# Kernel optimization log

Measured on AMD Instinct MI355X. Metric: run time of the kernel, lower is better.

Reference implementation:

```python
import jax, jax.numpy as jnp
import numpy as np

EMBED_DIM = 1024
NUM_HEADS = 16
HEAD_DIM = EMBED_DIM // NUM_HEADS
SCALING = HEAD_DIM ** (-0.5)
SEQ = 2048
BSZ = 2


def setup_inputs() -> dict:
    key = jax.random.key(0)
    ks = jax.random.split(key, 11)
    d = {
        "query": jax.random.normal(ks[0], (SEQ, BSZ, EMBED_DIM), dtype=jnp.float32),
        "key": jax.random.normal(ks[1], (SEQ, BSZ, EMBED_DIM), dtype=jnp.float32),
        "value": jax.random.normal(ks[2], (SEQ, BSZ, EMBED_DIM), dtype=jnp.float32),
        "bias_q": jax.random.normal(ks[3], (SEQ, EMBED_DIM), dtype=jnp.float32),
        "bias_k": jax.random.normal(ks[4], (SEQ, EMBED_DIM), dtype=jnp.float32),
        "bias_v": jax.random.normal(ks[5], (SEQ, EMBED_DIM), dtype=jnp.float32),
        # Linear weights (out, in); xavier-ish scale
        "Wq": jax.random.normal(ks[6], (EMBED_DIM, EMBED_DIM), dtype=jnp.float32) * (1.0 / np.sqrt(2 * EMBED_DIM)),
        "Wk": jax.random.normal(ks[7], (EMBED_DIM, EMBED_DIM), dtype=jnp.float32) * (1.0 / np.sqrt(2 * EMBED_DIM)),
        "Wv": jax.random.normal(ks[8], (EMBED_DIM, EMBED_DIM), dtype=jnp.float32) * (1.0 / np.sqrt(2 * EMBED_DIM)),
        "Wo": jax.random.normal(ks[9], (EMBED_DIM, EMBED_DIM), dtype=jnp.float32) * (1.0 / np.sqrt(EMBED_DIM)),
        "bo": jnp.zeros((EMBED_DIM,), dtype=jnp.float32),
    }
    return d


def reference(query, key, value, bias_q, bias_k, bias_v, Wq, Wk, Wv, Wo, bo):
    tgt_len, bsz, embed_dim = query.shape
    # self_attention=True: q, k, v all projected from `query`
    q = (query @ Wq.T + bias_q[:, None, :]) * SCALING   # [T,B,E]
    k = query @ Wk.T + bias_k[:, None, :]                # [T,B,E]
    v = query @ Wv.T + bias_v[:, None, :]                # [T,B,E]

    def split_heads(x):  # [T,B,E] -> [B*H, T, Dh]
        return x.reshape(tgt_len, bsz * NUM_HEADS, HEAD_DIM).transpose(1, 0, 2)

    q, k, v = split_heads(q), split_heads(k), split_heads(v)
    attn_weights = jnp.einsum('btd,bsd->bts', q, k)      # [B*H, T, S]
    attn_weights = jax.nn.softmax(attn_weights, axis=-1)
    attn = jnp.einsum('bts,bsd->btd', attn_weights, v)   # [B*H, T, Dh]
    attn = attn.transpose(1, 0, 2).reshape(tgt_len, bsz, embed_dim)
    attn = attn @ Wo.T + bo
    return (attn, attn_weights)
```

## Files before the change

### kernel.cpp

```cpp
#include <hip/hip_runtime.h>
#include <hip/hip_fp16.h>
#include <cmath>

#define SEQLEN 2048
#define BATCH 2
#define EMB 1024
#define NHEAD 16
#define DHEAD 64
#define NBH 32
#define NROWS 4096

typedef _Float16 f16;
typedef __attribute__((ext_vector_type(4))) _Float16 f16x4;
typedef __attribute__((ext_vector_type(8))) _Float16 f16x8;
typedef __attribute__((ext_vector_type(4))) float f32x4;

__device__ __forceinline__ void gload_lds16(const f16* g, f16* l) {
    __builtin_amdgcn_global_load_lds(
        (const __attribute__((address_space(1))) void*)g,
        (__attribute__((address_space(3))) void*)l, 16, 0, 0);
}

#define QN4 1048576
#define WN4 262144
__global__ __launch_bounds__(256) void cvt_all_kernel(
    const float* __restrict__ query, const float* __restrict__ w0,
    const float* __restrict__ w1, const float* __restrict__ w2,
    const float* __restrict__ w3,
    f16* __restrict__ xh, f16* __restrict__ o0, f16* __restrict__ o1,
    f16* __restrict__ o2, f16* __restrict__ o3)
{
    const int total = QN4 + 4 * WN4;
    for (int i = blockIdx.x * 256 + threadIdx.x; i < total; i += 2048 * 256) {
        const float* src; f16* dst; int off;
        if (i < QN4) { src = query; dst = xh; off = i; }
        else {
            int j = i - QN4;
            int sel = j >> 18;
            off = j & (WN4 - 1);
            switch (sel) {
                case 0: src = w0; dst = o0; break;
                case 1: src = w1; dst = o1; break;
                case 2: src = w2; dst = o2; break;
                default: src = w3; dst = o3; break;
            }
        }
        float4 v = reinterpret_cast<const float4*>(src)[off];
        f16x4 o = {(_Float16)v.x, (_Float16)v.y, (_Float16)v.z, (_Float16)v.w};
        reinterpret_cast<f16x4*>(dst)[off] = o;
    }
}

#define PBK 32

__global__ __launch_bounds__(256, 3) void proj_kernel(
    const f16* __restrict__ xh,
    const f16* __restrict__ Wqh, const f16* __restrict__ Wkh, const f16* __restrict__ Wvh,
    const float* __restrict__ bq, const float* __restrict__ bk, const float* __restrict__ bv,
    f16* __restrict__ qh, f16* __restrict__ kh, f16* __restrict__ vT)
{
    __shared__ __align__(16) f16 smem[16384];

    const int c0f = blockIdx.y * 128;
    const int mode = c0f >> 10;
    const int c0 = c0f & 1023;
    const f16* __restrict__ W = (mode == 0) ? Wqh : (mode == 1 ? Wkh : Wvh);
    const float* __restrict__ bias = (mode == 0) ? bq : (mode == 1 ? bk : bv);
    const int r0 = blockIdx.x * 128;
    const int w = threadIdx.x >> 6;
    const int lane = threadIdx.x & 63;
    const int lr = lane & 15, lg = lane >> 4;
    const int wr = w >> 1, wc = w & 1;

    const int cA0 = w * 64 + lane;
    const int cA1 = 256 + w * 64 + lane;
    const f16* gA0 = xh + (size_t)(r0 + (cA0 >> 2)) * EMB + (cA0 & 3) * 8;
    const f16* gA1 = xh + (size_t)(r0 + (cA1 >> 2)) * EMB + (cA1 & 3) * 8;
    const f16* gB0 = W + (size_t)(c0 + (cA0 >> 2)) * EMB + (cA0 & 3) * 8;
    const f16* gB1 = W + (size_t)(c0 + (cA1 >> 2)) * EMB + (cA1 & 3) * 8;
    const int lds0 = (w * 64) * 8;
    const int lds1 = (256 + w * 64) * 8;

    f32x4 acc[4][4] = {};
    int cur = 0;

    gload_lds16(gA0, smem + lds0);
    gload_lds16(gA1, smem + lds1);
    gload_lds16(gB0, smem + 8192 + lds0);
    gload_lds16(gB1, smem + 8192 + lds1);
    __syncthreads();

    for (int kt = 0; kt < EMB / PBK; ++kt) {
        if (kt + 1 < EMB / PBK) {
            const int ko = (kt + 1) * PBK;
            const int nxt = (cur ^ 1) * 4096;
            gload_lds16(gA0 + ko, smem + nxt + lds0);
            gload_lds16(gA1 + ko, smem + nxt + lds1);
            gload_lds16(gB0 + ko, smem + 8192 + nxt + lds0);
            gload_lds16(gB1 + ko, smem + 8192 + nxt + lds1);
        }
        const f16* Ac = smem + cur * 4096;
        const f16* Bc = smem + 8192 + cur * 4096;
        f16x8 a[4], b[4];
#pragma unroll
        for (int m = 0; m < 4; ++m)
            a[m] = *reinterpret_cast<const f16x8*>(
                &Ac[(wr * 64 + m * 16 + lr) * PBK + lg * 8]);
#pragma unroll
        for (int n = 0; n < 4; ++n)
            b[n] = *reinterpret_cast<const f16x8*>(
                &Bc[(wc * 64 + n * 16 + lr) * PBK + lg * 8]);
#pragma unroll
        for (int m = 0; m < 4; ++m)
#pragma unroll
            for (int n = 0; n < 4; ++n)
                acc[m][n] = __builtin_amdgcn_mfma_f32_16x16x32_f16(b[n], a[m], acc[m][n], 0, 0, 0);
        __syncthreads();
        cur ^= 1;
    }

    if (mode != 2) {
        f16* __restrict__ dst = (mode == 0) ? qh : kh;
        const float sc = (mode == 0) ? 0.125f : 1.0f;
#pragma unroll
        for (int m = 0; m < 4; ++m) {
            const int row = r0 + wr * 64 + m * 16 + lr;
            const int t = row >> 1, bb = row & 1;
#pragma unroll
            for (int n = 0; n < 4; ++n) {
                const int col0 = c0 + wc * 64 + n * 16 + lg * 4;
                float4 b4 = *reinterpret_cast<const float4*>(&bias[(size_t)t * EMB + col0]);
                f16x4 pk = {(_Float16)((acc[m][n][0] + b4.x) * sc),
                            (_Float16)((acc[m][n][1] + b4.y) * sc),
                            (_Float16)((acc[m][n][2] + b4.z) * sc),
                            (_Float16)((acc[m][n][3] + b4.w) * sc)};
                const int h = col0 >> 6, d0 = col0 & 63;
                const int bhi = bb * NHEAD + h;
                *reinterpret_cast<f16x4*>(
                    &dst[((size_t)bhi * SEQLEN + t) * DHEAD + d0]) = pk;
            }
        }
    } else {
        f16* T = smem;
#pragma unroll
        for (int p = 0; p < 2; ++p) {
            if (wr == p) {
#pragma unroll
                for (int m = 0; m < 4; ++m) {
                    const int row = r0 + p * 64 + m * 16 + lr;
                    const int t = row >> 1;
#pragma unroll
                    for (int n = 0; n < 4; ++n) {
                        const int ci0 = wc * 64 + n * 16 + lg * 4;
                        float4 b4 = *reinterpret_cast<const float4*>(
                            &bias[(size_t)t * EMB + c0 + ci0]);
                        f16x4 pk = {(_Float16)(acc[m][n][0] + b4.x),
                                    (_Float16)(acc[m][n][1] + b4.y),
                                    (_Float16)(acc[m][n][2] + b4.z),
                                    (_Float16)(acc[m][n][3] + b4.w)};
                        *reinterpret_cast<f16x4*>(&T[(m * 16 + lr) * 132 + ci0]) = pk;
                    }
                }
            }
            __syncthreads();
            {
                const int dd = threadIdx.x & 63;
                const int hh = (threadIdx.x >> 6) & 1;
                const int bb2 = threadIdx.x >> 7;
                const int bhi2 = bb2 * NHEAD + ((c0 + hh * 64) >> 6);
                const int tbase = (r0 + p * 64) >> 1;
                f16* __restrict__ vrow =
                    vT + ((size_t)bhi2 * 64 + (tbase >> 5)) * (DHEAD * 32) + dd * 32;
#pragma unroll
                for (int j8 = 0; j8 < 4; ++j8) {
                    f16x8 pk8;
#pragma unroll
                    for (int jj = 0; jj < 8; ++jj)
                        pk8[jj] = T[(bb2 + 2 * (j8 * 8 + jj)) * 132 + hh * 64 + dd];
                    *reinterpret_cast<f16x8*>(&vrow[j8 * 8]) = pk8;
                }
            }
            __syncthreads();
        }
    }
}

#define QBLK 16
#define SCHUNK 256
#define TPITCH 264
#define RPITCH 1040

__global__ __launch_bounds__(512, 4) void attn_kernel(
    const f16* __restrict__ qh, const f16* __restrict__ kh, const f16* __restrict__ vT,
    float* __restrict__ Pout, f16* __restrict__ ctx)
{
    __shared__ __align__(16) f16 tbuf[8][QBLK * TPITCH];
    __shared__ float lsum[QBLK][8];
    __shared__ float inv_l[QBLK];
    float* red = (float*)&tbuf[0][0];

    const int id = blockIdx.x;
    const int idx = id >> 3;
    const int bh = ((id & 7) << 2) + (idx >> 7);
    const int t0 = (idx & 127) * QBLK;

    const int w = threadIdx.x >> 6;
    const int lane = threadIdx.x & 63;
    const int lr = lane & 15, lg = lane >> 4;
    const int sbase = w * SCHUNK;

    const f16* __restrict__ qb = qh + (size_t)bh * SEQLEN * DHEAD;
    const f16* __restrict__ kb = kh + (size_t)bh * SEQLEN * DHEAD;
    const f16* __restrict__ vb = vT + (size_t)bh * DHEAD * SEQLEN;

    f16x8 qf[2];
#pragma unroll
    for (int kc = 0; kc < 2; ++kc)
        qf[kc] = *reinterpret_cast<const f16x8*>(
            qb + (size_t)(t0 + lr) * DHEAD + kc * 32 + lg * 8);

    f16x4 ev[16];
    float rowsum = 0.f;
#pragma unroll
    for (int st = 0; st < 16; ++st) {
        const f16* krow = kb + (size_t)(sbase + st * 16 + lr) * DHEAD;
        f16x8 kf0 = *reinterpret_cast<const f16x8*>(krow + lg * 8);
        f16x8 kf1 = *reinterpret_cast<const f16x8*>(krow + 32 + lg * 8);
        f32x4 sa = {};
        sa = __builtin_amdgcn_mfma_f32_16x16x32_f16(kf0, qf[0], sa, 0, 0, 0);
        sa = __builtin_amdgcn_mfma_f32_16x16x32_f16(kf1, qf[1], sa, 0, 0, 0);
        float ps = 0.f;
#pragma unroll
        for (int e = 0; e < 4; ++e) {
            float Ev = __expf(sa[e]) * 0.0625f;
            ev[st][e] = (_Float16)Ev;
            ps += Ev;
        }
        rowsum += ps;
    }

    {
        float v = rowsum;
        v += __shfl_xor(v, 16);
        v += __shfl_xor(v, 32);
        if (lg == 0) lsum[lr][w] = v;
    }

    f16* mybuf = &tbuf[w][0];
#pragma unroll
    for (int st = 0; st < 16; ++st)
        *reinterpret_cast<f16x4*>(&mybuf[lr * TPITCH + st * 16 + lg * 4]) = ev[st];

    __syncthreads();
    if (threadIdx.x < QBLK) {
        float s = 0.f;
#pragma unroll
        for (int i = 0; i < 8; ++i) s += lsum[threadIdx.x][i];
        inv_l[threadIdx.x] = 1.0f / s;
    }
    __syncthreads();

    float* __restrict__ Pt =
        Pout + (size_t)bh * SEQLEN * SEQLEN + (size_t)t0 * SEQLEN;
#pragma unroll
    for (int j = 0; j < 2; ++j) {
        const int t = w * 2 + j;
        const float inv = inv_l[t];
#pragma unroll
        for (int c = 0; c < 8; ++c) {
            f16x4 e4 = *reinterpret_cast<const f16x4*>(
                &tbuf[c][t * TPITCH + lane * 4]);
            f32x4 o = {(float)e4[0] * inv, (float)e4[1] * inv,
                       (float)e4[2] * inv, (float)e4[3] * inv};
            __builtin_nontemporal_store(o,
                reinterpret_cast<f32x4*>(&Pt[(size_t)t * SEQLEN + c * SCHUNK + lane * 4]));
        }
    }

    f32x4 accO[4] = {};
#pragma unroll
    for (int c = 0; c < 8; ++c) {
        f16x8 pa = *reinterpret_cast<const f16x8*>(&mybuf[lr * TPITCH + c * 32 + lg * 8]);
        const f16* vchunk = vb + (size_t)(w * 8 + c) * (DHEAD * 32);
#pragma unroll
        for (int dt = 0; dt < 4; ++dt) {
            f16x8 vf = *reinterpret_cast<const f16x8*>(
                vchunk + (dt * 16 + lr) * 32 + lg * 8);
            accO[dt] = __builtin_amdgcn_mfma_f32_16x16x32_f16(pa, vf, accO[dt], 0, 0, 0);
        }
    }
    __syncthreads();

#pragma unroll
    for (int dt = 0; dt < 4; ++dt)
#pragma unroll
        for (int e = 0; e < 4; ++e)
            red[(size_t)w * RPITCH + (lg * 4 + e) * 65 + dt * 16 + lr] = accO[dt][e];
    __syncthreads();

    const int b = bh >> 4, h = bh & 15;
    for (int o = threadIdx.x; o < QBLK * DHEAD; o += 512) {
        const int t = o >> 6, d = o & 63;
        float s = 0.f;
#pragma unroll
        for (int i = 0; i < 8; ++i) s += red[(size_t)i * RPITCH + t * 65 + d];
        s *= inv_l[t];
        ctx[(size_t)((t0 + t) * BATCH + b) * EMB + h * DHEAD + d] = (f16)s;
    }
}

__global__ __launch_bounds__(256, 4) void oproj_kernel(
    const f16* __restrict__ ctx, const f16* __restrict__ Woh,
    const float* __restrict__ bo, float* __restrict__ out)
{
    __shared__ __align__(16) f16 smem[12288];
    const int r0 = blockIdx.x * 64;
    const int c0 = blockIdx.y * 128;
    const int w = threadIdx.x >> 6;
    const int lane = threadIdx.x & 63;
    const int lr = lane & 15, lg = lane >> 4;
    const int wr = w >> 1, wc = w & 1;

    const int cA = threadIdx.x;
    const f16* gA = ctx + (size_t)(r0 + (cA >> 2)) * EMB + (cA & 3) * 8;
    const f16* gB0 = Woh + (size_t)(c0 + (cA >> 2)) * EMB + (cA & 3) * 8;
    const f16* gB1 = Woh + (size_t)(c0 + 64 + (cA >> 2)) * EMB + (cA & 3) * 8;
    const int ldsA = (w * 64) * 8;
    const int ldsB0 = (w * 64) * 8;
    const int ldsB1 = (256 + w * 64) * 8;

    f32x4 acc[2][4] = {};
    int cur = 0;

    gload_lds16(gA, smem + ldsA);
    gload_lds16(gB0, smem + 4096 + ldsB0);
    gload_lds16(gB1, smem + 4096 + ldsB1);
    __syncthreads();

    for (int kt = 0; kt < EMB / PBK; ++kt) {
        if (kt + 1 < EMB / PBK) {
            const int ko = (kt + 1) * PBK;
            const int nxtA = (cur ^ 1) * 2048;
            const int nxtB = 4096 + (cur ^ 1) * 4096;
            gload_lds16(gA + ko, smem + nxtA + ldsA);
            gload_lds16(gB0 + ko, smem + nxtB + ldsB0);
            gload_lds16(gB1 + ko, smem + nxtB + ldsB1);
        }
        const f16* Ac = smem + cur * 2048;
        const f16* Bc = smem + 4096 + cur * 4096;
        f16x8 a[2], b[4];
#pragma unroll
        for (int m = 0; m < 2; ++m)
            a[m] = *reinterpret_cast<const f16x8*>(
                &Ac[(wr * 32 + m * 16 + lr) * PBK + lg * 8]);
#pragma unroll
        for (int n = 0; n < 4; ++n)
            b[n] = *reinterpret_cast<const f16x8*>(
                &Bc[(wc * 64 + n * 16 + lr) * PBK + lg * 8]);
#pragma unroll
        for (int m = 0; m < 2; ++m)
#pragma unroll
            for (int n = 0; n < 4; ++n)
                acc[m][n] = __builtin_amdgcn_mfma_f32_16x16x32_f16(b[n], a[m], acc[m][n], 0, 0, 0);
        __syncthreads();
        cur ^= 1;
    }

#pragma unroll
    for (int m = 0; m < 2; ++m) {
        const int row = r0 + wr * 32 + m * 16 + lr;
#pragma unroll
        for (int n = 0; n < 4; ++n) {
            const int col0 = c0 + wc * 64 + n * 16 + lg * 4;
            float4 b4 = *reinterpret_cast<const float4*>(&bo[col0]);
            f32x4 o = {acc[m][n][0] + b4.x, acc[m][n][1] + b4.y,
                       acc[m][n][2] + b4.z, acc[m][n][3] + b4.w};
            __builtin_nontemporal_store(o,
                reinterpret_cast<f32x4*>(&out[(size_t)row * EMB + col0]));
        }
    }
}

extern "C" void kernel_launch(void* const* d_in, const int* in_sizes, int n_in,
                              void* d_out, int out_size, void* d_ws, size_t ws_size,
                              hipStream_t stream) {
    const float* query = (const float*)d_in[0];
    const float* bq = (const float*)d_in[3];
    const float* bk = (const float*)d_in[4];
    const float* bv = (const float*)d_in[5];
    const float* Wq = (const float*)d_in[6];
    const float* Wk = (const float*)d_in[7];
    const float* Wv = (const float*)d_in[8];
    const float* Wo = (const float*)d_in[9];
    const float* bo = (const float*)d_in[10];

    char* ws = (char*)d_ws;
    f16* xh  = (f16*)(ws);
    f16* Wqh = (f16*)(ws + ( 8u << 20));
    f16* Wkh = (f16*)(ws + (10u << 20));
    f16* Wvh = (f16*)(ws + (12u << 20));
    f16* Woh = (f16*)(ws + (14u << 20));
    f16* qhp = (f16*)(ws + (16u << 20));
    f16* khp = (f16*)(ws + (24u << 20));
    f16* vTp = (f16*)(ws + (32u << 20));
    f16* ctx = (f16*)(ws + (40u << 20));

    float* outA = (float*)d_out;
    float* outP = (float*)d_out + (size_t)SEQLEN * BATCH * EMB;

    cvt_all_kernel<<<2048, 256, 0, stream>>>(query, Wq, Wk, Wv, Wo,
                                             xh, Wqh, Wkh, Wvh, Woh);

    proj_kernel<<<dim3(NROWS / 128, 3072 / 128), 256, 0, stream>>>(
        xh, Wqh, Wkh, Wvh, bq, bk, bv, qhp, khp, vTp);

    attn_kernel<<<SEQLEN / QBLK * NBH, 512, 0, stream>>>(qhp, khp, vTp, outP, ctx);

    oproj_kernel<<<dim3(NROWS / 64, EMB / 128), 256, 0, stream>>>(ctx, Woh, bo, outA);
}
```

Before: 264.6 us.

## Process 32 query rows per attention block with 16 waves sharing K/V loads

Doubles the query tile per block to 32 rows and splits the key range across 16 waves of 128 keys each, so every loaded K and V fragment feeds two MFMA query tiles. This is meant to cut global K/V reload traffic per query row. It raises LDS usage to about 139 KB and uses 1024-thread blocks, which limits occupancy to one block per CU. The cross-wave reduction of the output grows to 16 partials.

Result: faster. 228.1 us (median of 2 runs) (-13.8%).

```diff
diff --git a/kernel.cpp b/kernel.cpp
--- a/kernel.cpp
+++ b/kernel.cpp
@@ -185,24 +185,24 @@
     }
 }
 
-#define QBLK 16
-#define SCHUNK 256
-#define TPITCH 264
-#define RPITCH 1040
-
-__global__ __launch_bounds__(512, 4) void attn_kernel(
+#define QBLK 32
+#define SCHUNK 128
+#define TP 136
+#define RP 2080
+
+__global__ __launch_bounds__(1024, 1) void attn_kernel(
     const f16* __restrict__ qh, const f16* __restrict__ kh, const f16* __restrict__ vT,
     float* __restrict__ Pout, f16* __restrict__ ctx)
 {
-    __shared__ __align__(16) f16 tbuf[8][QBLK * TPITCH];
-    __shared__ float lsum[QBLK][8];
+    __shared__ __align__(16) f16 tbuf[16][QBLK * TP];
+    __shared__ float lsum[QBLK][16];
     __shared__ float inv_l[QBLK];
     float* red = (float*)&tbuf[0][0];
 
     const int id = blockIdx.x;
     const int idx = id >> 3;
-    const int bh = ((id & 7) << 2) + (idx >> 7);
-    const int t0 = (idx & 127) * QBLK;
+    const int bh = ((id & 7) << 2) + (idx >> 6);
+    const int t0 = (idx & 63) * QBLK;
 
     const int w = threadIdx.x >> 6;
     const int lane = threadIdx.x & 63;
@@ -213,49 +213,58 @@
     const f16* __restrict__ kb = kh + (size_t)bh * SEQLEN * DHEAD;
     const f16* __restrict__ vb = vT + (size_t)bh * DHEAD * SEQLEN;
 
-    f16x8 qf[2];
-#pragma unroll
-    for (int kc = 0; kc < 2; ++kc)
-        qf[kc] = *reinterpret_cast<const f16x8*>(
-            qb + (size_t)(t0 + lr) * DHEAD + kc * 32 + lg * 8);
-
-    f16x4 ev[16];
-    float rowsum = 0.f;
-#pragma unroll
-    for (int st = 0; st < 16; ++st) {
+    f16x8 qf[2][2];
+#pragma unroll
+    for (int tt = 0; tt < 2; ++tt)
+#pragma unroll
+        for (int kc = 0; kc < 2; ++kc)
+            qf[tt][kc] = *reinterpret_cast<const f16x8*>(
+                qb + (size_t)(t0 + tt * 16 + lr) * DHEAD + kc * 32 + lg * 8);
+
+    f16x4 ev[2][8];
+    float rowsum[2] = {0.f, 0.f};
+#pragma unroll
+    for (int st = 0; st < 8; ++st) {
         const f16* krow = kb + (size_t)(sbase + st * 16 + lr) * DHEAD;
         f16x8 kf0 = *reinterpret_cast<const f16x8*>(krow + lg * 8);
         f16x8 kf1 = *reinterpret_cast<const f16x8*>(krow + 32 + lg * 8);
-        f32x4 sa = {};
-        sa = __builtin_amdgcn_mfma_f32_16x16x32_f16(kf0, qf[0], sa, 0, 0, 0);
-        sa = __builtin_amdgcn_mfma_f32_16x16x32_f16(kf1, qf[1], sa, 0, 0, 0);
-        float ps = 0.f;
-#pragma unroll
-        for (int e = 0; e < 4; ++e) {
-            float Ev = __expf(sa[e]) * 0.0625f;
-            ev[st][e] = (_Float16)Ev;
-            ps += Ev;
-        }
-        rowsum += ps;
-    }
-
-    {
-        float v = rowsum;
+#pragma unroll
+        for (int tt = 0; tt < 2; ++tt) {
+            f32x4 sa = {};
+            sa = __builtin_amdgcn_mfma_f32_16x16x32_f16(kf0, qf[tt][0], sa, 0, 0, 0);
+            sa = __builtin_amdgcn_mfma_f32_16x16x32_f16(kf1, qf[tt][1], sa, 0, 0, 0);
+            float ps = 0.f;
+#pragma unroll
+            for (int e = 0; e < 4; ++e) {
+                float Ev = __expf(sa[e]) * 0.0625f;
+                ev[tt][st][e] = (_Float16)Ev;
+                ps += Ev;
+            }
+            rowsum[tt] += ps;
+        }
+    }
+
+#pragma unroll
+    for (int tt = 0; tt < 2; ++tt) {
+        float v = rowsum[tt];
         v += __shfl_xor(v, 16);
         v += __shfl_xor(v, 32);
-        if (lg == 0) lsum[lr][w] = v;
+        if (lg == 0) lsum[tt * 16 + lr][w] = v;
     }
 
     f16* mybuf = &tbuf[w][0];
 #pragma unroll
-    for (int st = 0; st < 16; ++st)
-        *reinterpret_cast<f16x4*>(&mybuf[lr * TPITCH + st * 16 + lg * 4]) = ev[st];
+    for (int tt = 0; tt < 2; ++tt)
+#pragma unroll
+        for (int st = 0; st < 8; ++st)
+            *reinterpret_cast<f16x4*>(
+                &mybuf[(tt * 16 + lr) * TP + st * 16 + lg * 4]) = ev[tt][st];
 
     __syncthreads();
     if (threadIdx.x < QBLK) {
         float s = 0.f;
 #pragma unroll
-        for (int i = 0; i < 8; ++i) s += lsum[threadIdx.x][i];
+        for (int i = 0; i < 16; ++i) s += lsum[threadIdx.x][i];
         inv_l[threadIdx.x] = 1.0f / s;
     }
     __syncthreads();
@@ -267,43 +276,50 @@
         const int t = w * 2 + j;
         const float inv = inv_l[t];
 #pragma unroll
-        for (int c = 0; c < 8; ++c) {
+        for (int cc = 0; cc < 8; ++cc) {
+            const int chunk = cc * 2 + (lane >> 5);
+            const int col = (lane & 31) * 4;
             f16x4 e4 = *reinterpret_cast<const f16x4*>(
-                &tbuf[c][t * TPITCH + lane * 4]);
+                &tbuf[chunk][t * TP + col]);
             f32x4 o = {(float)e4[0] * inv, (float)e4[1] * inv,
                        (float)e4[2] * inv, (float)e4[3] * inv};
             __builtin_nontemporal_store(o,
-                reinterpret_cast<f32x4*>(&Pt[(size_t)t * SEQLEN + c * SCHUNK + lane * 4]));
-        }
-    }
-
-    f32x4 accO[4] = {};
-#pragma unroll
-    for (int c = 0; c < 8; ++c) {
-        f16x8 pa = *reinterpret_cast<const f16x8*>(&mybuf[lr * TPITCH + c * 32 + lg * 8]);
-        const f16* vchunk = vb + (size_t)(w * 8 + c) * (DHEAD * 32);
+                reinterpret_cast<f32x4*>(&Pt[(size_t)t * SEQLEN + cc * 256 + lane * 4]));
+        }
+    }
+
+    f32x4 accO[2][4] = {};
+#pragma unroll
+    for (int c = 0; c < 4; ++c) {
+        f16x8 pa0 = *reinterpret_cast<const f16x8*>(&mybuf[lr * TP + c * 32 + lg * 8]);
+        f16x8 pa1 = *reinterpret_cast<const f16x8*>(&mybuf[(16 + lr) * TP + c * 32 + lg * 8]);
+        const f16* vchunk = vb + (size_t)(w * 4 + c) * (DHEAD * 32);
 #pragma unroll
         for (int dt = 0; dt < 4; ++dt) {
             f16x8 vf = *reinterpret_cast<const f16x8*>(
                 vchunk + (dt * 16 + lr) * 32 + lg * 8);
-            accO[dt] = __builtin_amdgcn_mfma_f32_16x16x32_f16(pa, vf, accO[dt], 0, 0, 0);
-        }
-    }
-    __syncthreads();
-
-#pragma unroll
-    for (int dt = 0; dt < 4; ++dt)
-#pragma unroll
-        for (int e = 0; e < 4; ++e)
-            red[(size_t)w * RPITCH + (lg * 4 + e) * 65 + dt * 16 + lr] = accO[dt][e];
+            accO[0][dt] = __builtin_amdgcn_mfma_f32_16x16x32_f16(pa0, vf, accO[0][dt], 0, 0, 0);
+            accO[1][dt] = __builtin_amdgcn_mfma_f32_16x16x32_f16(pa1, vf, accO[1][dt], 0, 0, 0);
+        }
+    }
+    __syncthreads();
+
+#pragma unroll
+    for (int tt = 0; tt < 2; ++tt)
+#pragma unroll
+        for (int dt = 0; dt < 4; ++dt)
+#pragma unroll
+            for (int e = 0; e < 4; ++e)
+                red[(size_t)w * RP + (tt * 16 + lg * 4 + e) * 65 + dt * 16 + lr] =
+                    accO[tt][dt][e];
     __syncthreads();
 
     const int b = bh >> 4, h = bh & 15;
-    for (int o = threadIdx.x; o < QBLK * DHEAD; o += 512) {
+    for (int o = threadIdx.x; o < QBLK * DHEAD; o += 1024) {
         const int t = o >> 6, d = o & 63;
         float s = 0.f;
 #pragma unroll
-        for (int i = 0; i < 8; ++i) s += red[(size_t)i * RPITCH + t * 65 + d];
+        for (int i = 0; i < 16; ++i) s += red[(size_t)i * RP + t * 65 + d];
         s *= inv_l[t];
         ctx[(size_t)((t0 + t) * BATCH + b) * EMB + h * DHEAD + d] = (f16)s;
     }
@@ -414,7 +430,7 @@
     proj_kernel<<<dim3(NROWS / 128, 3072 / 128), 256, 0, stream>>>(
         xh, Wqh, Wkh, Wvh, bq, bk, bv, qhp, khp, vTp);
 
-    attn_kernel<<<SEQLEN / QBLK * NBH, 512, 0, stream>>>(qhp, khp, vTp, outP, ctx);
+    attn_kernel<<<SEQLEN / QBLK * NBH, 1024, 0, stream>>>(qhp, khp, vTp, outP, ctx);
 
     oproj_kernel<<<dim3(NROWS / 64, EMB / 128), 256, 0, stream>>>(ctx, Woh, bo, outA);
 }
```
